# Optimization experiments

Measured on AMD Instinct MI355X. Metric: run time of the kernel, lower is better.

The kernel has to match this reference:

```python
import jax, jax.numpy as jnp
import numpy as np

N_NODES = 100000
N_EDGES = 1600000
D_IN = 128
D_HID = 128
D_OUT = 128
N_LAYERS = 4


def setup_inputs() -> dict:
    key = jax.random.key(0)
    ks = jax.random.split(key, 8)
    x = jax.random.normal(ks[0], (N_NODES, D_IN), dtype=jnp.float32)
    edge_index = jax.random.randint(ks[1], (2, N_EDGES), 0, N_NODES, dtype=jnp.int64)
    s = 1.0 / np.sqrt(D_IN)
    # All layers are 128->128, so stack weights: [L, in, out]
    W_lin = jax.random.uniform(ks[2], (N_LAYERS, D_IN, D_HID), minval=-s, maxval=s, dtype=jnp.float32)
    W_film = jax.random.uniform(ks[3], (N_LAYERS, D_IN, 2 * D_HID), minval=-s, maxval=s, dtype=jnp.float32)
    b_film = jax.random.uniform(ks[4], (N_LAYERS, 2 * D_HID), minval=-s, maxval=s, dtype=jnp.float32)
    W_skip = jax.random.uniform(ks[5], (N_LAYERS, D_IN, D_HID), minval=-s, maxval=s, dtype=jnp.float32)
    W_fskip = jax.random.uniform(ks[6], (N_LAYERS, D_IN, 2 * D_HID), minval=-s, maxval=s, dtype=jnp.float32)
    return {"x": x, "edge_index": edge_index, "W_lin": W_lin, "W_film": W_film,
            "b_film": b_film, "W_skip": W_skip, "W_fskip": W_fskip}


def _film_conv(x, src, dst, deg_inv, W_l, W_f, b_f, W_s, W_fs, c):
    # skip path: FiLM-modulated self transform
    bg_s = x @ W_fs                       # [N, 2C], no bias
    beta_s, gamma_s = bg_s[:, :c], bg_s[:, c:]
    out = jax.nn.relu(gamma_s * (x @ W_s) + beta_s)
    # message path: FiLM params from target node, features from source node
    bg = x @ W_f + b_f                    # [N, 2C]
    beta, gamma = bg[:, :c], bg[:, c:]
    h = x @ W_l                           # [N, C]
    msg = jax.nn.relu(gamma[dst] * h[src] + beta[dst])  # [E, C]
    agg = jax.ops.segment_sum(msg, dst, num_segments=x.shape[0]) * deg_inv  # mean aggr
    return out + agg


def reference(x, edge_index, W_lin, W_film, b_film, W_skip, W_fskip):
    src, dst = edge_index[0], edge_index[1]
    n = x.shape[0]
    deg = jax.ops.segment_sum(jnp.ones((src.shape[0],), x.dtype), dst, num_segments=n)
    deg_inv = (1.0 / jnp.maximum(deg, 1.0))[:, None]   # clamp(min=1) like PyG mean
    for l in range(N_LAYERS):
        x = _film_conv(x, src, dst, deg_inv, W_lin[l], W_film[l], b_film[l],
                       W_skip[l], W_fskip[l], D_HID)
        if l < N_LAYERS - 1:
            x = jax.nn.relu(x)
    return x
```

## Files before the change

### kernel.cpp

```cpp
#include <hip/hip_runtime.h>
#include <hip/hip_bf16.h>

#define N_NODES 100000
#define N_PAD   100096
#define N_EDGES 1600000
#define NXCD    8
#define NRANGE  ((N_NODES + NXCD - 1) / NXCD)
#define NSLICE  256

typedef __bf16 bf16x8 __attribute__((ext_vector_type(8)));
typedef float  f32x4  __attribute__((ext_vector_type(4)));

__device__ __forceinline__ void gload16(const void* g, void* s) {
    __builtin_amdgcn_global_load_lds(
        (const __attribute__((address_space(1))) unsigned int*)g,
        (__attribute__((address_space(3))) unsigned int*)s, 16, 0, 0);
}

__device__ __forceinline__ float2 bf2f(unsigned p) {
    float2 r;
    union { unsigned u; float f; } a, b;
    a.u = p << 16;
    b.u = p & 0xffff0000u;
    r.x = a.f; r.y = b.f;
    return r;
}
__device__ __forceinline__ unsigned f2bf2(float x, float y) {
    unsigned lo = (unsigned)__builtin_bit_cast(unsigned short, __float2bfloat16(x));
    unsigned hi = (unsigned)__builtin_bit_cast(unsigned short, __float2bfloat16(y));
    return lo | (hi << 16);
}

__global__ void detect_kernel(const unsigned* __restrict__ e, int* __restrict__ flag) {
    __shared__ int nz;
    if (threadIdx.x == 0) nz = 0;
    __syncthreads();
    int local = 0;
    for (int i = threadIdx.x; i < 1024; i += blockDim.x)
        if (e[2 * i + 1] != 0) local = 1;
    if (local) atomicOr(&nz, 1);
    __syncthreads();
    if (threadIdx.x == 0) *flag = (nz == 0) ? 1 : 0;
}

__device__ __forceinline__ int edge_at(const unsigned* __restrict__ e, long idx, int is64) {
    return (int)(is64 ? e[2 * idx] : e[idx]);
}

__global__ void hist_kernel(const unsigned* __restrict__ e, const int* __restrict__ flag,
                            int* __restrict__ counts) {
    int i = blockIdx.x * blockDim.x + threadIdx.x;
    if (i >= N_EDGES) return;
    int is64 = *flag;
    int d = edge_at(e, (long)N_EDGES + i, is64);
    atomicAdd(&counts[d], 1);
}

__global__ void scan1_kernel(const int* __restrict__ counts, int* __restrict__ blockSums) {
    __shared__ int red[256];
    int base = blockIdx.x * 1024;
    int sum = 0;
    for (int i = threadIdx.x; i < 1024; i += 256) {
        int idx = base + i;
        sum += (idx < N_NODES) ? counts[idx] : 0;
    }
    red[threadIdx.x] = sum;
    __syncthreads();
    for (int s = 128; s > 0; s >>= 1) {
        if (threadIdx.x < s) red[threadIdx.x] += red[threadIdx.x + s];
        __syncthreads();
    }
    if (threadIdx.x == 0) blockSums[blockIdx.x] = red[0];
}

__global__ void scan2_kernel(int* __restrict__ blockSums, int nb, int* __restrict__ row_ptr) {
    int run = 0;
    for (int i = 0; i < nb; ++i) { int v = blockSums[i]; blockSums[i] = run; run += v; }
    row_ptr[N_NODES] = run;
}

__global__ void scan3_kernel(const int* __restrict__ counts, const int* __restrict__ blockSums,
                             int* __restrict__ row_ptr, int* __restrict__ cursor,
                             float* __restrict__ deg_inv) {
    __shared__ int lds[256];
    int base = blockIdx.x * 1024;
    int t = threadIdx.x;
    int v[4];
    int s = 0;
    for (int i = 0; i < 4; ++i) {
        int idx = base + t * 4 + i;
        v[i] = (idx < N_NODES) ? counts[idx] : 0;
        s += v[i];
    }
    lds[t] = s;
    __syncthreads();
    for (int off = 1; off < 256; off <<= 1) {
        int add = (t >= off) ? lds[t - off] : 0;
        __syncthreads();
        lds[t] += add;
        __syncthreads();
    }
    int excl = lds[t] - s + blockSums[blockIdx.x];
    for (int i = 0; i < 4; ++i) {
        int idx = base + t * 4 + i;
        if (idx < N_NODES) {
            row_ptr[idx] = excl;
            cursor[idx]  = excl;
            deg_inv[idx] = 1.0f / fmaxf((float)v[i], 1.0f);
            excl += v[i];
        }
    }
}

__global__ __launch_bounds__(256) void fill2_kernel(
    const unsigned* __restrict__ e, const int* __restrict__ flag,
    int* __restrict__ cursor, int* __restrict__ csr_src) {
    const int r     = blockIdx.x & (NXCD - 1);
    const int slice = blockIdx.x >> 3;
    const int lo = r * NRANGE;
    const int hi = min(lo + NRANGE, N_NODES);
    const int is64 = *flag;
    const int per = (N_EDGES + NSLICE - 1) / NSLICE;
    const int i0 = slice * per;
    const int i1 = min(i0 + per, N_EDGES);
    for (int i = i0 + (int)threadIdx.x; i < i1; i += 256) {
        int d = edge_at(e, (long)N_EDGES + i, is64);
        if (d >= lo && d < hi) {
            int s = edge_at(e, (long)i, is64);
            int pos = atomicAdd(&cursor[d], 1);
            csr_src[pos] = s;
        }
    }
}

__global__ void bt_prep_kernel(const float* __restrict__ Wl, const float* __restrict__ Wf,
                               const float* __restrict__ Ws, const float* __restrict__ Wfs,
                               __hip_bfloat16* __restrict__ Bt) {
    int idx = blockIdx.x * 256 + threadIdx.x;
    if (idx >= 4 * 768 * 128) return;
    int k   = idx % 128;
    int row = (idx / 128) % 768;
    int lay = idx / (128 * 768);
    float w;
    if (row < 128) {
        w = Wl[(size_t)lay * 16384 + k * 128 + row];
    } else if (row < 384) {
        w = Wf[(size_t)lay * 32768 + k * 256 + (row - 128)];
    } else {
        int rr = row - 384;
        int g = rr >> 4, within = rr & 15;
        int kind = g % 3;
        int c = (g / 3) * 16 + within;
        if (kind == 0)      w = Ws [(size_t)lay * 16384 + k * 128 + c];
        else if (kind == 1) w = Wfs[(size_t)lay * 32768 + k * 256 + c];
        else                w = Wfs[(size_t)lay * 32768 + k * 256 + 128 + c];
    }
    Bt[idx] = __float2bfloat16(w);
}

__global__ void cast_kernel(const float* __restrict__ x, unsigned* __restrict__ A2) {
    long i = (long)blockIdx.x * 256 + threadIdx.x;
    if (i >= (long)N_NODES * 64) return;
    float2 v = ((const float2*)x)[i];
    A2[i] = f2bf2(v.x, v.y);
}

__global__ __launch_bounds__(256, 2) void fused_gemm_kernel(
    const __hip_bfloat16* __restrict__ A,
    const __hip_bfloat16* __restrict__ Bt,
    const float* __restrict__ bfilm,
    __hip_bfloat16* __restrict__ hbuf,
    __hip_bfloat16* __restrict__ bgbuf,
    __hip_bfloat16* __restrict__ skbh)
{
    __shared__ alignas(16) unsigned char lds_raw[32768];
    unsigned char* ldsA = lds_raw;
    unsigned char* ldsB = lds_raw + 16384;

    const int t  = threadIdx.x;
    const int mt = blockIdx.x / 7;
    const int jt = blockIdx.x % 7;
    const long node0 = (long)mt * 128;
    const int w  = t >> 6, l = t & 63;
    const int wm = w >> 1, wn = w & 1;
    const int lr = l & 15;
    const int kq16 = (l >> 4) << 4;
    const int sw = (lr & 7) << 4;

    const int sr  = t >> 3;
    const int scb = (t & 7) << 4;
    const int scbs = scb ^ ((sr & 7) << 4);

    const char* Abase = (const char*)A;

    if (jt < 3) {
        const char* Bbase = (const char*)Bt + (size_t)(jt * 128) * 256;
        f32x4 acc[4][4];
        #pragma unroll
        for (int mi = 0; mi < 4; ++mi)
            #pragma unroll
            for (int ni = 0; ni < 4; ++ni)
                #pragma unroll
                for (int j = 0; j < 4; ++j) acc[mi][ni][j] = 0.f;

        #pragma unroll
        for (int ks = 0; ks < 2; ++ks) {
            const int k0 = ks * 64;
            #pragma unroll
            for (int i = 0; i < 4; ++i) {
                const int r = (i << 5) + sr;
                gload16(Abase + (node0 + r) * 256 + (size_t)k0 * 2 + scbs,
                        ldsA + (((i << 8) + t) << 4));
                gload16(Bbase + (size_t)r * 256 + (size_t)k0 * 2 + scbs,
                        ldsB + (((i << 8) + t) << 4));
            }
            __syncthreads();

            #pragma unroll
            for (int kh = 0; kh < 2; ++kh) {
                const int kbs = ((kh << 6) + kq16) ^ sw;
                bf16x8 af[4], bfr[4];
                #pragma unroll
                for (int mi = 0; mi < 4; ++mi)
                    af[mi] = *(const bf16x8*)(ldsA + (wm * 64 + mi * 16 + lr) * 128 + kbs);
                #pragma unroll
                for (int ni = 0; ni < 4; ++ni)
                    bfr[ni] = *(const bf16x8*)(ldsB + (wn * 64 + ni * 16 + lr) * 128 + kbs);
                #pragma unroll
                for (int mi = 0; mi < 4; ++mi)
                    #pragma unroll
                    for (int ni = 0; ni < 4; ++ni)
                        acc[mi][ni] = __builtin_amdgcn_mfma_f32_16x16x32_bf16(
                            af[mi], bfr[ni], acc[mi][ni], 0, 0, 0);
            }
            __syncthreads();
        }

        const int col = lr;
        const int rb  = (l >> 4) << 2;
        if (jt == 0) {
            #pragma unroll
            for (int mi = 0; mi < 4; ++mi)
                #pragma unroll
                for (int ni = 0; ni < 4; ++ni) {
                    const int n = wn * 64 + ni * 16 + col;
                    #pragma unroll
                    for (int j = 0; j < 4; ++j) {
                        long node = node0 + wm * 64 + mi * 16 + rb + j;
                        if (node < N_NODES)
                            hbuf[node * 128 + n] = __float2bfloat16(acc[mi][ni][j]);
                    }
                }
        } else {
            const int c0 = (jt - 1) * 128;
            #pragma unroll
            for (int mi = 0; mi < 4; ++mi)
                #pragma unroll
                for (int ni = 0; ni < 4; ++ni) {
                    const int n = wn * 64 + ni * 16 + col;
                    const float bb = bfilm[c0 + n];
                    #pragma unroll
                    for (int j = 0; j < 4; ++j) {
                        long node = node0 + wm * 64 + mi * 16 + rb + j;
                        if (node < N_NODES)
                            bgbuf[node * 256 + c0 + n] = __float2bfloat16(acc[mi][ni][j] + bb);
                    }
                }
        }
    } else {
        const int jt2 = jt - 3;
        const char* Bbase = (const char*)Bt + (size_t)(384 + jt2 * 96) * 256;
        f32x4 acc[4][3];
        #pragma unroll
        for (int mi = 0; mi < 4; ++mi)
            #pragma unroll
            for (int ni = 0; ni < 3; ++ni)
                #pragma unroll
                for (int j = 0; j < 4; ++j) acc[mi][ni][j] = 0.f;

        #pragma unroll
        for (int ks = 0; ks < 2; ++ks) {
            const int k0 = ks * 64;
            #pragma unroll
            for (int i = 0; i < 4; ++i) {
                const int r = (i << 5) + sr;
                gload16(Abase + (node0 + r) * 256 + (size_t)k0 * 2 + scbs,
                        ldsA + (((i << 8) + t) << 4));
            }
            #pragma unroll
            for (int i = 0; i < 3; ++i) {
                const int r = (i << 5) + sr;
                gload16(Bbase + (size_t)r * 256 + (size_t)k0 * 2 + scbs,
                        ldsB + (((i << 8) + t) << 4));
            }
            __syncthreads();

            #pragma unroll
            for (int kh = 0; kh < 2; ++kh) {
                const int kbs = ((kh << 6) + kq16) ^ sw;
                bf16x8 af[4], bfr[3];
                #pragma unroll
                for (int mi = 0; mi < 4; ++mi)
                    af[mi] = *(const bf16x8*)(ldsA + (wm * 64 + mi * 16 + lr) * 128 + kbs);
                #pragma unroll
                for (int ni = 0; ni < 3; ++ni)
                    bfr[ni] = *(const bf16x8*)(ldsB + (wn * 48 + ni * 16 + lr) * 128 + kbs);
                #pragma unroll
                for (int mi = 0; mi < 4; ++mi)
                    #pragma unroll
                    for (int ni = 0; ni < 3; ++ni)
                        acc[mi][ni] = __builtin_amdgcn_mfma_f32_16x16x32_bf16(
                            af[mi], bfr[ni], acc[mi][ni], 0, 0, 0);
            }
            __syncthreads();
        }

        const int c  = (2 * jt2 + wn) * 16 + lr;
        const int rb = (l >> 4) << 2;
        #pragma unroll
        for (int mi = 0; mi < 4; ++mi)
            #pragma unroll
            for (int j = 0; j < 4; ++j) {
                long node = node0 + wm * 64 + mi * 16 + rb + j;
                if (node < N_NODES) {
                    float o = fmaxf(acc[mi][2][j] * acc[mi][0][j] + acc[mi][1][j], 0.f);
                    skbh[node * 128 + c] = __float2bfloat16(o);
                }
            }
    }
}

__global__ __launch_bounds__(256) void agg_kernel(
    const uint2* __restrict__ h22,
    const uint2* __restrict__ bgu2,
    const int* __restrict__ row_ptr, const int* __restrict__ csr_src,
    const float* __restrict__ deg_inv,
    const uint2* __restrict__ sku2,
    uint2* __restrict__ An2,
    float4* __restrict__ fo4)
{
    const int t = threadIdx.x;
    const int v = blockIdx.x * 4 + (t >> 6);
    const int l = t & 63;
    const int half = l >> 5;
    const unsigned c = l & 31;

    const uint2 bu = bgu2[(size_t)v * 64 + c];
    const uint2 gu = bgu2[(size_t)v * 64 + 32 + c];
    const float2 be01 = bf2f(bu.x), be23 = bf2f(bu.y);
    const float2 ga01 = bf2f(gu.x), ga23 = bf2f(gu.y);
    const float dinv = deg_inv[v];

    const int b = row_ptr[v];
    const int e = row_ptr[v + 1];
    const int ne = e - b;
    const int npair = ne >> 1;

    f32x4 ac0 = {0,0,0,0}, ac1 = {0,0,0,0}, ac2 = {0,0,0,0}, ac3 = {0,0,0,0};

    const int* cp = csr_src + b + half;

#define ACC(A_, P_) do {                                   \
        float2 h01 = bf2f((P_).x), h23 = bf2f((P_).y);     \
        (A_)[0] += fmaxf(ga01.x * h01.x + be01.x, 0.f);    \
        (A_)[1] += fmaxf(ga01.y * h01.y + be01.y, 0.f);    \
        (A_)[2] += fmaxf(ga23.x * h23.x + be23.x, 0.f);    \
        (A_)[3] += fmaxf(ga23.y * h23.y + be23.y, 0.f);    \
    } while (0)

    int pi = 0;
    for (; pi + 4 <= npair; pi += 4) {
        const int i0 = 2 * pi;
        const unsigned s0 = (unsigned)cp[i0];
        const unsigned s1 = (unsigned)cp[i0 + 2];
        const unsigned s2 = (unsigned)cp[i0 + 4];
        const unsigned s3 = (unsigned)cp[i0 + 6];
        const uint2 p0 = h22[s0 * 32u + c];
        const uint2 p1 = h22[s1 * 32u + c];
        const uint2 p2 = h22[s2 * 32u + c];
        const uint2 p3 = h22[s3 * 32u + c];
        ACC(ac0, p0); ACC(ac1, p1); ACC(ac2, p2); ACC(ac3, p3);
    }
    for (; pi < npair; ++pi) {
        const unsigned s0 = (unsigned)cp[2 * pi];
        const uint2 p0 = h22[s0 * 32u + c];
        ACC(ac0, p0);
    }
    if ((ne & 1) && half == 0) {
        const unsigned s0 = (unsigned)csr_src[e - 1];
        const uint2 p0 = h22[s0 * 32u + c];
        ACC(ac1, p0);
    }
#undef ACC

    float r0 = (ac0[0] + ac1[0]) + (ac2[0] + ac3[0]);
    float r1 = (ac0[1] + ac1[1]) + (ac2[1] + ac3[1]);
    float r2 = (ac0[2] + ac1[2]) + (ac2[2] + ac3[2]);
    float r3 = (ac0[3] + ac1[3]) + (ac2[3] + ac3[3]);
    r0 += __shfl_xor(r0, 32);
    r1 += __shfl_xor(r1, 32);
    r2 += __shfl_xor(r2, 32);
    r3 += __shfl_xor(r3, 32);

    const uint2 sk = sku2[(size_t)v * 32 + c];
    const float2 s01 = bf2f(sk.x), s23 = bf2f(sk.y);
    const float o0 = s01.x + r0 * dinv;
    const float o1 = s01.y + r1 * dinv;
    const float o2 = s23.x + r2 * dinv;
    const float o3 = s23.y + r3 * dinv;

    if (half == 0) {
        if (An2) {
            An2[(size_t)v * 32 + c] = make_uint2(f2bf2(o0, o1), f2bf2(o2, o3));
        } else {
            fo4[(size_t)v * 32 + c] = make_float4(o0, o1, o2, o3);
        }
    }
}

extern "C" void kernel_launch(void* const* d_in, const int* in_sizes, int n_in,
                              void* d_out, int out_size, void* d_ws, size_t ws_size,
                              hipStream_t stream) {
    const float*    x_in    = (const float*)d_in[0];
    const unsigned* eidx    = (const unsigned*)d_in[1];
    const float*    W_lin   = (const float*)d_in[2];
    const float*    W_film  = (const float*)d_in[3];
    const float*    b_film  = (const float*)d_in[4];
    const float*    W_skip  = (const float*)d_in[5];
    const float*    W_fskip = (const float*)d_in[6];
    float*          out     = (float*)d_out;

    char* ws = (char*)d_ws;
    size_t off = 0;
    auto alloc = [&](size_t bytes) -> void* {
        void* p = ws + off;
        off = (off + bytes + 255) & ~(size_t)255;
        return p;
    };
    int*   flag      = (int*)alloc(4);
    int*   counts    = (int*)alloc((size_t)N_NODES * 4);
    int*   row_ptr   = (int*)alloc((size_t)(N_NODES + 1) * 4);
    int*   cursor    = (int*)alloc((size_t)N_NODES * 4);
    int*   blockSums = (int*)alloc(128 * 4);
    float* deg_inv   = (float*)alloc((size_t)N_NODES * 4);
    int*   csr_src   = (int*)alloc((size_t)N_EDGES * 4);
    __hip_bfloat16* Abuf  = (__hip_bfloat16*)alloc((size_t)N_PAD * 128 * 2);
    __hip_bfloat16* BtAll = (__hip_bfloat16*)alloc((size_t)4 * 768 * 128 * 2);
    __hip_bfloat16* hbuf  = (__hip_bfloat16*)alloc((size_t)N_NODES * 128 * 2);
    __hip_bfloat16* bgbuf = (__hip_bfloat16*)alloc((size_t)N_NODES * 256 * 2);
    __hip_bfloat16* skbh  = (__hip_bfloat16*)alloc((size_t)N_NODES * 128 * 2);
    (void)ws_size; (void)in_sizes; (void)n_in; (void)out_size;

    const int NB_SCAN = (N_NODES + 1023) / 1024;
    const int EB = (N_EDGES + 255) / 256;

    hipMemsetAsync(counts, 0, (size_t)N_NODES * 4, stream);
    detect_kernel<<<1, 256, 0, stream>>>(eidx, flag);
    hist_kernel<<<EB, 256, 0, stream>>>(eidx, flag, counts);
    scan1_kernel<<<NB_SCAN, 256, 0, stream>>>(counts, blockSums);
    scan2_kernel<<<1, 1, 0, stream>>>(blockSums, NB_SCAN, row_ptr);
    scan3_kernel<<<NB_SCAN, 256, 0, stream>>>(counts, blockSums, row_ptr, cursor, deg_inv);
    fill2_kernel<<<NXCD * NSLICE, 256, 0, stream>>>(eidx, flag, cursor, csr_src);

    cast_kernel<<<(N_NODES * 64 + 255) / 256, 256, 0, stream>>>(x_in, (unsigned*)Abuf);
    bt_prep_kernel<<<(4 * 768 * 128 + 255) / 256, 256, 0, stream>>>(
        W_lin, W_film, W_skip, W_fskip, BtAll);

    const int MT = N_PAD / 128;
    const int AGG_B = N_NODES / 4;
    for (int l = 0; l < 4; ++l) {
        const __hip_bfloat16* Bt_l = BtAll + (size_t)l * 768 * 128;
        fused_gemm_kernel<<<MT * 7, 256, 0, stream>>>(
            Abuf, Bt_l, b_film + (size_t)l * 256, hbuf, bgbuf, skbh);
        agg_kernel<<<AGG_B, 256, 0, stream>>>(
            (const uint2*)hbuf, (const uint2*)bgbuf,
            row_ptr, csr_src, deg_inv, (const uint2*)skbh,
            (l < 3) ? (uint2*)Abuf : (uint2*)nullptr,
            (l == 3) ? (float4*)out : (float4*)nullptr);
    }
}
```

Baseline: 659.2 us.

## Compute all seven GEMM column tiles per block with A kept in registers

The GEMM grid changes from 7 blocks per 128-row tile to one block per tile. Each block loads the whole 128x128 A tile into LDS once and holds its fragments in registers, then streams the B column blocks through LDS, reloading the next one after each tile is computed. This removes the sevenfold re-read of A from global memory, but each block now does its column tiles serially and launches only about 782 blocks. It also uses 64KB of LDS and more registers, which may lower occupancy. Separately, the aggregation gather loop is unrolled to 8 edges so more loads are in flight.

Measured after the change: 787.5 us. 1.19x slower.

```diff
diff --git a/kernel.cpp b/kernel.cpp
--- a/kernel.cpp
+++ b/kernel.cpp
@@ -165,7 +165,7 @@
     A2[i] = f2bf2(v.x, v.y);
 }
 
-__global__ __launch_bounds__(256, 2) void fused_gemm_kernel(
+__global__ __launch_bounds__(256, 2) void layer_gemm_kernel(
     const __hip_bfloat16* __restrict__ A,
     const __hip_bfloat16* __restrict__ Bt,
     const float* __restrict__ bfilm,
@@ -173,28 +173,49 @@
     __hip_bfloat16* __restrict__ bgbuf,
     __hip_bfloat16* __restrict__ skbh)
 {
-    __shared__ alignas(16) unsigned char lds_raw[32768];
-    unsigned char* ldsA = lds_raw;
-    unsigned char* ldsB = lds_raw + 16384;
-
-    const int t  = threadIdx.x;
-    const int mt = blockIdx.x / 7;
-    const int jt = blockIdx.x % 7;
-    const long node0 = (long)mt * 128;
+    __shared__ alignas(16) unsigned char ldsA[32768];
+    __shared__ alignas(16) unsigned char ldsB[32768];
+
+    const int t = threadIdx.x;
+    const long node0 = (long)blockIdx.x * 128;
     const int w  = t >> 6, l = t & 63;
     const int wm = w >> 1, wn = w & 1;
     const int lr = l & 15;
     const int kq16 = (l >> 4) << 4;
     const int sw = (lr & 7) << 4;
 
-    const int sr  = t >> 3;
-    const int scb = (t & 7) << 4;
-    const int scbs = scb ^ ((sr & 7) << 4);
+    const int srow = t >> 4;
+    const int scol = (t & 15) << 4;
+    const int scbs = scol ^ ((srow & 7) << 4);
 
     const char* Abase = (const char*)A;
-
-    if (jt < 3) {
-        const char* Bbase = (const char*)Bt + (size_t)(jt * 128) * 256;
+    const char* Bbase = (const char*)Bt;
+
+    auto stageB = [&](int rowbase, int passes) {
+        for (int i = 0; i < passes; ++i)
+            gload16(Bbase + (size_t)(rowbase + (i << 4) + srow) * 256 + scbs,
+                    ldsB + (i << 12) + t * 16);
+    };
+
+    #pragma unroll
+    for (int i = 0; i < 8; ++i)
+        gload16(Abase + (node0 + (i << 4) + srow) * 256 + scbs,
+                ldsA + (i << 12) + t * 16);
+    stageB(0, 8);
+    __syncthreads();
+
+    bf16x8 af[4][4];
+    #pragma unroll
+    for (int kh = 0; kh < 4; ++kh)
+        #pragma unroll
+        for (int mi = 0; mi < 4; ++mi)
+            af[kh][mi] = *(const bf16x8*)(
+                ldsA + (wm * 64 + mi * 16 + lr) * 256 + (((kh << 6) + kq16) ^ sw));
+
+    const int col = lr;
+    const int rb  = (l >> 4) << 2;
+
+    for (int c = 0; c < 3; ++c) {
         f32x4 acc[4][4];
         #pragma unroll
         for (int mi = 0; mi < 4; ++mi)
@@ -204,41 +225,24 @@
                 for (int j = 0; j < 4; ++j) acc[mi][ni][j] = 0.f;
 
         #pragma unroll
-        for (int ks = 0; ks < 2; ++ks) {
-            const int k0 = ks * 64;
-            #pragma unroll
-            for (int i = 0; i < 4; ++i) {
-                const int r = (i << 5) + sr;
-                gload16(Abase + (node0 + r) * 256 + (size_t)k0 * 2 + scbs,
-                        ldsA + (((i << 8) + t) << 4));
-                gload16(Bbase + (size_t)r * 256 + (size_t)k0 * 2 + scbs,
-                        ldsB + (((i << 8) + t) << 4));
-            }
-            __syncthreads();
-
-            #pragma unroll
-            for (int kh = 0; kh < 2; ++kh) {
-                const int kbs = ((kh << 6) + kq16) ^ sw;
-                bf16x8 af[4], bfr[4];
-                #pragma unroll
-                for (int mi = 0; mi < 4; ++mi)
-                    af[mi] = *(const bf16x8*)(ldsA + (wm * 64 + mi * 16 + lr) * 128 + kbs);
+        for (int kh = 0; kh < 4; ++kh) {
+            const int kbs = ((kh << 6) + kq16) ^ sw;
+            bf16x8 bfr[4];
+            #pragma unroll
+            for (int ni = 0; ni < 4; ++ni)
+                bfr[ni] = *(const bf16x8*)(ldsB + (wn * 64 + ni * 16 + lr) * 256 + kbs);
+            #pragma unroll
+            for (int mi = 0; mi < 4; ++mi)
                 #pragma unroll
                 for (int ni = 0; ni < 4; ++ni)
-                    bfr[ni] = *(const bf16x8*)(ldsB + (wn * 64 + ni * 16 + lr) * 128 + kbs);
-                #pragma unroll
-                for (int mi = 0; mi < 4; ++mi)
-                    #pragma unroll
-                    for (int ni = 0; ni < 4; ++ni)
-                        acc[mi][ni] = __builtin_amdgcn_mfma_f32_16x16x32_bf16(
-                            af[mi], bfr[ni], acc[mi][ni], 0, 0, 0);
-            }
-            __syncthreads();
-        }
-
-        const int col = lr;
-        const int rb  = (l >> 4) << 2;
-        if (jt == 0) {
+                    acc[mi][ni] = __builtin_amdgcn_mfma_f32_16x16x32_bf16(
+                        af[kh][mi], bfr[ni], acc[mi][ni], 0, 0, 0);
+        }
+        __syncthreads();
+        if (c < 2) stageB((c + 1) * 128, 8);
+        else       stageB(384, 6);
+
+        if (c == 0) {
             #pragma unroll
             for (int mi = 0; mi < 4; ++mi)
                 #pragma unroll
@@ -252,7 +256,7 @@
                     }
                 }
         } else {
-            const int c0 = (jt - 1) * 128;
+            const int c0 = (c - 1) * 128;
             #pragma unroll
             for (int mi = 0; mi < 4; ++mi)
                 #pragma unroll
@@ -267,9 +271,10 @@
                     }
                 }
         }
-    } else {
-        const int jt2 = jt - 3;
-        const char* Bbase = (const char*)Bt + (size_t)(384 + jt2 * 96) * 256;
+        __syncthreads();
+    }
+
+    for (int j2 = 0; j2 < 4; ++j2) {
         f32x4 acc[4][3];
         #pragma unroll
         for (int mi = 0; mi < 4; ++mi)
@@ -279,44 +284,23 @@
                 for (int j = 0; j < 4; ++j) acc[mi][ni][j] = 0.f;
 
         #pragma unroll
-        for (int ks = 0; ks < 2; ++ks) {
-            const int k0 = ks * 64;
-            #pragma unroll
-            for (int i = 0; i < 4; ++i) {
-                const int r = (i << 5) + sr;
-                gload16(Abase + (node0 + r) * 256 + (size_t)k0 * 2 + scbs,
-                        ldsA + (((i << 8) + t) << 4));
-            }
-            #pragma unroll
-            for (int i = 0; i < 3; ++i) {
-                const int r = (i << 5) + sr;
-                gload16(Bbase + (size_t)r * 256 + (size_t)k0 * 2 + scbs,
-                        ldsB + (((i << 8) + t) << 4));
-            }
-            __syncthreads();
-
-            #pragma unroll
-            for (int kh = 0; kh < 2; ++kh) {
-                const int kbs = ((kh << 6) + kq16) ^ sw;
-                bf16x8 af[4], bfr[3];
-                #pragma unroll
-                for (int mi = 0; mi < 4; ++mi)
-                    af[mi] = *(const bf16x8*)(ldsA + (wm * 64 + mi * 16 + lr) * 128 + kbs);
+        for (int kh = 0; kh < 4; ++kh) {
+            const int kbs = ((kh << 6) + kq16) ^ sw;
+            bf16x8 bfr[3];
+            #pragma unroll
+            for (int ni = 0; ni < 3; ++ni)
+                bfr[ni] = *(const bf16x8*)(ldsB + (wn * 48 + ni * 16 + lr) * 256 + kbs);
+            #pragma unroll
+            for (int mi = 0; mi < 4; ++mi)
                 #pragma unroll
                 for (int ni = 0; ni < 3; ++ni)
-                    bfr[ni] = *(const bf16x8*)(ldsB + (wn * 48 + ni * 16 + lr) * 128 + kbs);
-                #pragma unroll
-                for (int mi = 0; mi < 4; ++mi)
-                    #pragma unroll
-                    for (int ni = 0; ni < 3; ++ni)
-                        acc[mi][ni] = __builtin_amdgcn_mfma_f32_16x16x32_bf16(
-                            af[mi], bfr[ni], acc[mi][ni], 0, 0, 0);
-            }
-            __syncthreads();
-        }
-
-        const int c  = (2 * jt2 + wn) * 16 + lr;
-        const int rb = (l >> 4) << 2;
+                    acc[mi][ni] = __builtin_amdgcn_mfma_f32_16x16x32_bf16(
+                        af[kh][mi], bfr[ni], acc[mi][ni], 0, 0, 0);
+        }
+        __syncthreads();
+        if (j2 < 3) stageB(384 + (j2 + 1) * 96, 6);
+
+        const int cc = (2 * j2 + wn) * 16 + lr;
         #pragma unroll
         for (int mi = 0; mi < 4; ++mi)
             #pragma unroll
@@ -324,9 +308,10 @@
                 long node = node0 + wm * 64 + mi * 16 + rb + j;
                 if (node < N_NODES) {
                     float o = fmaxf(acc[mi][2][j] * acc[mi][0][j] + acc[mi][1][j], 0.f);
-                    skbh[node * 128 + c] = __float2bfloat16(o);
+                    skbh[node * 128 + cc] = __float2bfloat16(o);
                 }
             }
+        if (j2 < 3) __syncthreads();
     }
 }
 
@@ -369,17 +354,24 @@
     } while (0)
 
     int pi = 0;
+    for (; pi + 8 <= npair; pi += 8) {
+        unsigned s[8];
+        uint2 p[8];
+        #pragma unroll
+        for (int u = 0; u < 8; ++u) s[u] = (unsigned)cp[2 * (pi + u)];
+        #pragma unroll
+        for (int u = 0; u < 8; ++u) p[u] = h22[s[u] * 32u + c];
+        ACC(ac0, p[0]); ACC(ac1, p[1]); ACC(ac2, p[2]); ACC(ac3, p[3]);
+        ACC(ac0, p[4]); ACC(ac1, p[5]); ACC(ac2, p[6]); ACC(ac3, p[7]);
+    }
     for (; pi + 4 <= npair; pi += 4) {
-        const int i0 = 2 * pi;
-        const unsigned s0 = (unsigned)cp[i0];
-        const unsigned s1 = (unsigned)cp[i0 + 2];
-        const unsigned s2 = (unsigned)cp[i0 + 4];
-        const unsigned s3 = (unsigned)cp[i0 + 6];
-        const uint2 p0 = h22[s0 * 32u + c];
-        const uint2 p1 = h22[s1 * 32u + c];
-        const uint2 p2 = h22[s2 * 32u + c];
-        const uint2 p3 = h22[s3 * 32u + c];
-        ACC(ac0, p0); ACC(ac1, p1); ACC(ac2, p2); ACC(ac3, p3);
+        unsigned s[4];
+        uint2 p[4];
+        #pragma unroll
+        for (int u = 0; u < 4; ++u) s[u] = (unsigned)cp[2 * (pi + u)];
+        #pragma unroll
+        for (int u = 0; u < 4; ++u) p[u] = h22[s[u] * 32u + c];
+        ACC(ac0, p[0]); ACC(ac1, p[1]); ACC(ac2, p[2]); ACC(ac3, p[3]);
     }
     for (; pi < npair; ++pi) {
         const unsigned s0 = (unsigned)cp[2 * pi];
@@ -470,7 +462,7 @@
     const int AGG_B = N_NODES / 4;
     for (int l = 0; l < 4; ++l) {
         const __hip_bfloat16* Bt_l = BtAll + (size_t)l * 768 * 128;
-        fused_gemm_kernel<<<MT * 7, 256, 0, stream>>>(
+        layer_gemm_kernel<<<MT, 256, 0, stream>>>(
             Abuf, Bt_l, b_film + (size_t)l * 256, hbuf, bgbuf, skbh);
         agg_kernel<<<AGG_B, 256, 0, stream>>>(
             (const uint2*)hbuf, (const uint2*)bgbuf,
```
